# Optimization experiments

Hardware: AMD Instinct MI355X
Metric: run time of the kernel (lower is better)

The kernel has to match this reference:

```python
import jax, jax.numpy as jnp
import numpy as np

B, N, D, L = 4, 256, 512, 3  # batch, seq_len, input_dim, n_layer


def setup_inputs() -> dict:
    key = jax.random.key(0)
    ks = jax.random.split(key, 12)
    s = 0.02
    return {
        "x": jax.random.normal(ks[0], (B, N, D), dtype=jnp.float32),
        # Highway: L layers, each a gate Linear(D,D) and transform Linear(D,D)
        "hw_gate_w": jax.random.normal(ks[1], (L, D, D), dtype=jnp.float32) * s,
        "hw_gate_b": jnp.zeros((L, D), dtype=jnp.float32),
        "hw_tr_w": jax.random.normal(ks[2], (L, D, D), dtype=jnp.float32) * s,
        "hw_tr_b": jnp.zeros((L, D), dtype=jnp.float32),
        # link_weight MLP: Linear(2D,D) -> ReLU -> [Linear(D,D) -> ReLU]*(L-2) -> Linear(D,1) -> Sigmoid
        "lw0_w": jax.random.normal(ks[3], (D, 2 * D), dtype=jnp.float32) * s,
        "lw0_b": jnp.zeros((D,), dtype=jnp.float32),
        "lw1_w": jax.random.normal(ks[4], (D, D), dtype=jnp.float32) * s,
        "lw1_b": jnp.zeros((D,), dtype=jnp.float32),
        "lwo_w": jax.random.normal(ks[5], (1, D), dtype=jnp.float32) * s,
        "lwo_b": jnp.zeros((1,), dtype=jnp.float32),
    }


def _highway(x, gw, gb, tw, tb):
    # standard highway: y = g * relu(Wt x + bt) + (1 - g) * x, g = sigmoid(Wg x + bg)
    for i in range(gw.shape[0]):
        g = jax.nn.sigmoid(jnp.einsum('bnd,ed->bne', x, gw[i]) + gb[i])
        t = jax.nn.relu(jnp.einsum('bnd,ed->bne', x, tw[i]) + tb[i])
        x = g * t + (1.0 - g) * x
    return x


def reference(x, hw_gate_w, hw_gate_b, hw_tr_w, hw_tr_b,
              lw0_w, lw0_b, lw1_w, lw1_b, lwo_w, lwo_b):
    d = x.shape[-1]
    h = _highway(x, hw_gate_w, hw_gate_b, hw_tr_w, hw_tr_b)  # [B,N,D]
    # Fused pairwise-concat + first Linear: cat(h_i, h_j) @ W0.T ==
    # h_i @ W0[:, :D].T + h_j @ W0[:, D:].T  (avoids the [B,N*N,2D] tensor)
    a = jnp.einsum('bnd,ed->bne', h, lw0_w[:, :d])  # uses m1 (row i)
    b = jnp.einsum('bnd,ed->bne', h, lw0_w[:, d:])  # uses m2 (col j)
    z = jax.nn.relu(a[:, :, None, :] + b[:, None, :, :] + lw0_b)  # [B,N,N,D]
    # (dropout is identity in eval mode)
    z = jax.nn.relu(jnp.einsum('bijd,ed->bije', z, lw1_w) + lw1_b)  # n_layer-2 == 1 hidden layer
    out = jax.nn.sigmoid(jnp.einsum('bijd,d->bij', z, lwo_w[0]) + lwo_b[0])
    return out  # [B,N,N]
```

## Files before the change

### kernel.cpp

```cpp
#include <hip/hip_runtime.h>
#include <hip/hip_bf16.h>

#define BB 4
#define NN 256
#define DD 512

using short8   = __attribute__((ext_vector_type(8))) short;
using f32x4    = __attribute__((ext_vector_type(4))) float;
using uint32x4 = __attribute__((ext_vector_type(4))) unsigned int;

__device__ __forceinline__ unsigned short f2bf(float f) {
    unsigned int u = __float_as_uint(f);
    unsigned int r = (u + 0x7fffu + ((u >> 16) & 1u)) >> 16;
    return (unsigned short)r;
}

__device__ __forceinline__ unsigned cvtpk(float lo, float hi) {
    unsigned r;
    asm("v_cvt_pk_bf16_f32 %0, %1, %2" : "=v"(r) : "v"(lo), "v"(hi));
    return r;
}

template <int ROWS, int NW>
__device__ __forceinline__ void stage_rows(const unsigned short* src, int stride,
                                           short* dst, int tid) {
    int wave = tid >> 6, lane = tid & 63;
#pragma unroll
    for (int c = 0; c < ROWS / (8 * NW); ++c) {
        int rbase = (c * NW + wave) * 8;
        int row   = rbase + (lane >> 3);
        int slot  = (lane & 7) ^ (row & 7);
        const unsigned short* g = src + (size_t)row * stride + slot * 8;
        __builtin_amdgcn_global_load_lds(
            (const __attribute__((address_space(1))) void*)g,
            (__attribute__((address_space(3))) void*)(dst + rbase * 64),
            16, 0, 0);
    }
}

__device__ __forceinline__ short8 read_frag(const short* T, int rowBase, int k2) {
    int lane = threadIdx.x & 63;
    int row  = rowBase + (lane & 15);
    int slot = ((k2 * 4) + (lane >> 4)) ^ (row & 7);
    return *(const short8*)(T + row * 64 + slot * 8);
}

__global__ void prep_kernel(const float* __restrict__ x,
                            const float* __restrict__ gw, const float* __restrict__ tw,
                            const float* __restrict__ w0, const float* __restrict__ w1,
                            float* __restrict__ h0_f32, unsigned short* __restrict__ h0_bf,
                            unsigned short* __restrict__ wg_bf, unsigned short* __restrict__ wt_bf,
                            unsigned short* __restrict__ w0c_bf, unsigned short* __restrict__ w1_bf) {
    const int S_X = BB * NN * DD;
    const int S_W = 3 * DD * DD;
    const int S_W0 = 2 * DD * DD;
    const int S_W1 = DD * DD;
    int total = S_X + S_W + S_W + S_W0 + S_W1;
    for (int idx = blockIdx.x * blockDim.x + threadIdx.x; idx < total;
         idx += gridDim.x * blockDim.x) {
        int t = idx;
        if (t < S_X) { float v = x[t]; h0_f32[t] = v; h0_bf[t] = f2bf(v); continue; }
        t -= S_X;
        if (t < S_W) { wg_bf[t] = f2bf(gw[t]); continue; }
        t -= S_W;
        if (t < S_W) { wt_bf[t] = f2bf(tw[t]); continue; }
        t -= S_W;
        if (t < S_W0) {
            int e = t >> 9, d = t & 511;
            float v = (e < DD) ? w0[e * (2 * DD) + d] : w0[(e - DD) * (2 * DD) + DD + d];
            w0c_bf[t] = f2bf(v); continue;
        }
        t -= S_W0;
        w1_bf[t] = f2bf(w1[t]);
    }
}

__global__ __launch_bounds__(256) void highway_kernel(
        const float* __restrict__ h_in, const unsigned short* __restrict__ hbf_in,
        const unsigned short* __restrict__ wg_bf, const unsigned short* __restrict__ wt_bf,
        const float* __restrict__ gb, const float* __restrict__ tb,
        float* __restrict__ h_out, unsigned short* __restrict__ hbf_out) {
    __shared__ short ht[128 * 64];
    __shared__ short wgt[128 * 64];
    __shared__ short wtt[128 * 64];
    int tid = threadIdx.x, lane = tid & 63, wave = tid >> 6;
    int mt = blockIdx.x >> 2, et = blockIdx.x & 3;
    int m0 = mt * 128, e0 = et * 128;
    int wm = wave >> 1, we = wave & 1;
    f32x4 gacc[4][4] = {}, tacc[4][4] = {};
    for (int ks = 0; ks < 8; ++ks) {
        int d0 = ks * 64;
        __syncthreads();
        stage_rows<128, 4>(hbf_in + (size_t)m0 * DD + d0, DD, ht, tid);
        stage_rows<128, 4>(wg_bf + (size_t)e0 * DD + d0, DD, wgt, tid);
        stage_rows<128, 4>(wt_bf + (size_t)e0 * DD + d0, DD, wtt, tid);
        __syncthreads();
#pragma unroll
        for (int k2 = 0; k2 < 2; ++k2) {
            short8 af[4], bg[4], bt[4];
#pragma unroll
            for (int f = 0; f < 4; ++f) af[f] = read_frag(ht, wm * 64 + f * 16, k2);
#pragma unroll
            for (int f = 0; f < 4; ++f) bg[f] = read_frag(wgt, we * 64 + f * 16, k2);
#pragma unroll
            for (int f = 0; f < 4; ++f) bt[f] = read_frag(wtt, we * 64 + f * 16, k2);
#pragma unroll
            for (int fm = 0; fm < 4; ++fm)
#pragma unroll
                for (int fn = 0; fn < 4; ++fn) {
                    gacc[fm][fn] = __builtin_amdgcn_mfma_f32_16x16x32_bf16(af[fm], bg[fn], gacc[fm][fn], 0, 0, 0);
                    tacc[fm][fn] = __builtin_amdgcn_mfma_f32_16x16x32_bf16(af[fm], bt[fn], tacc[fm][fn], 0, 0, 0);
                }
        }
    }
#pragma unroll
    for (int fm = 0; fm < 4; ++fm)
#pragma unroll
        for (int fn = 0; fn < 4; ++fn) {
            int e = e0 + we * 64 + fn * 16 + (lane & 15);
            float gbe = gb[e], tbe = tb[e];
#pragma unroll
            for (int r = 0; r < 4; ++r) {
                int m = m0 + wm * 64 + fm * 16 + (lane >> 4) * 4 + r;
                float g = 1.f / (1.f + __expf(-(gacc[fm][fn][r] + gbe)));
                float tv = tacc[fm][fn][r] + tbe; tv = tv > 0.f ? tv : 0.f;
                float ho = h_in[(size_t)m * DD + e];
                float hn = g * tv + (1.f - g) * ho;
                h_out[(size_t)m * DD + e] = hn;
                hbf_out[(size_t)m * DD + e] = f2bf(hn);
            }
        }
}

__global__ __launch_bounds__(256) void ab_kernel(
        const unsigned short* __restrict__ hbf, const unsigned short* __restrict__ w0c_bf,
        const float* __restrict__ lw0_b,
        float* __restrict__ a_out, float* __restrict__ b_out) {
    __shared__ short ht[128 * 64];
    __shared__ short wt_[128 * 64];
    int tid = threadIdx.x, lane = tid & 63, wave = tid >> 6;
    int mt = blockIdx.x >> 3, et = blockIdx.x & 7;
    int m0 = mt * 128, e0 = et * 128;
    int wm = wave >> 1, we = wave & 1;
    f32x4 acc[4][4] = {};
    for (int ks = 0; ks < 8; ++ks) {
        __syncthreads();
        stage_rows<128, 4>(hbf + (size_t)m0 * DD + ks * 64, DD, ht, tid);
        stage_rows<128, 4>(w0c_bf + (size_t)e0 * DD + ks * 64, DD, wt_, tid);
        __syncthreads();
#pragma unroll
        for (int k2 = 0; k2 < 2; ++k2) {
            short8 af[4], bf_[4];
#pragma unroll
            for (int f = 0; f < 4; ++f) af[f] = read_frag(ht, wm * 64 + f * 16, k2);
#pragma unroll
            for (int f = 0; f < 4; ++f) bf_[f] = read_frag(wt_, we * 64 + f * 16, k2);
#pragma unroll
            for (int fm = 0; fm < 4; ++fm)
#pragma unroll
                for (int fn = 0; fn < 4; ++fn)
                    acc[fm][fn] = __builtin_amdgcn_mfma_f32_16x16x32_bf16(af[fm], bf_[fn], acc[fm][fn], 0, 0, 0);
        }
    }
#pragma unroll
    for (int fm = 0; fm < 4; ++fm)
#pragma unroll
        for (int fn = 0; fn < 4; ++fn) {
            int e = e0 + we * 64 + fn * 16 + (lane & 15);
#pragma unroll
            for (int r = 0; r < 4; ++r) {
                int m = m0 + wm * 64 + fm * 16 + (lane >> 4) * 4 + r;
                float v = acc[fm][fn][r];
                if (e < DD) a_out[(size_t)m * DD + e] = v + lw0_b[e];
                else        b_out[(size_t)m * DD + (e - DD)] = v;
            }
        }
}


#define Z_LOADS(K)                                                            \
    {                                                                         \
        const int dl_ = (K) * 64 + s * 8;                                     \
        alo = *(const f32x4*)(arow + dl_);                                    \
        ahi = *(const f32x4*)(arow + dl_ + 4);                                \
        const float* b0_ = brow + (size_t)rr * DD + dl_;                      \
        const float* b1_ = brow + (size_t)(64 + rr) * DD + dl_;               \
        b0lo = *(const f32x4*)b0_; b0hi = *(const f32x4*)(b0_ + 4);           \
        b1lo = *(const f32x4*)b1_; b1hi = *(const f32x4*)(b1_ + 4);           \
    }

#define Z_MATH()                                                              \
    {                                                                         \
        zw0[0] = cvtpk(fmaxf(alo[0] + b0lo[0], 0.f), fmaxf(alo[1] + b0lo[1], 0.f)); \
        zw0[1] = cvtpk(fmaxf(alo[2] + b0lo[2], 0.f), fmaxf(alo[3] + b0lo[3], 0.f)); \
        zw0[2] = cvtpk(fmaxf(ahi[0] + b0hi[0], 0.f), fmaxf(ahi[1] + b0hi[1], 0.f)); \
        zw0[3] = cvtpk(fmaxf(ahi[2] + b0hi[2], 0.f), fmaxf(ahi[3] + b0hi[3], 0.f)); \
        zw1[0] = cvtpk(fmaxf(alo[0] + b1lo[0], 0.f), fmaxf(alo[1] + b1lo[1], 0.f)); \
        zw1[1] = cvtpk(fmaxf(alo[2] + b1lo[2], 0.f), fmaxf(alo[3] + b1lo[3], 0.f)); \
        zw1[2] = cvtpk(fmaxf(ahi[0] + b1hi[0], 0.f), fmaxf(ahi[1] + b1hi[1], 0.f)); \
        zw1[3] = cvtpk(fmaxf(ahi[2] + b1hi[2], 0.f), fmaxf(ahi[3] + b1hi[3], 0.f)); \
    }

#define Z_WRITE()                                                             \
    {                                                                         \
        *(uint32x4*)(zs + rr * 64 + ((s ^ (rr & 7)) * 8)) = zw0;              \
        const int r1_ = 64 + rr;                                              \
        *(uint32x4*)(zs + r1_ * 64 + ((s ^ (r1_ & 7)) * 8)) = zw1;            \
    }

__global__ __launch_bounds__(512, 2) void pair_kernel(
        const float* __restrict__ a_f32, const float* __restrict__ b_f32,
        const unsigned short* __restrict__ w1_bf,
        const float* __restrict__ lw1_b, const float* __restrict__ lwo_w,
        const float* __restrict__ lwo_b, float* __restrict__ out) {
    __shared__ short ws[2][512 * 64];
    __shared__ short zs[128 * 64];
    int tid = threadIdx.x, lane = tid & 63, wave = tid >> 6;
    int bid = blockIdx.x;
    int bb = bid >> 9, i = (bid >> 1) & 255, j0 = (bid & 1) * 128;
    const float* arow = a_f32 + (size_t)(bb * NN + i) * DD;
    const float* brow = b_f32 + (size_t)(bb * NN + j0) * DD;
    int s = tid & 7, rr = tid >> 3;
    int we = wave;

    f32x4 acc[8][4] = {};
    uint32x4 zw0, zw1;
    f32x4 alo, ahi, b0lo, b0hi, b1lo, b1hi;

    Z_LOADS(0)
    Z_MATH()
    stage_rows<512, 8>(w1_bf, DD, ws[0], tid);

#pragma unroll
    for (int k = 0; k < 8; ++k) {
        __builtin_amdgcn_s_barrier();
        __builtin_amdgcn_sched_barrier(0);
        Z_WRITE()
        if (k < 7) {
            Z_LOADS(k + 1)
            stage_rows<512, 8>(w1_bf + (size_t)(k + 1) * 64, DD, ws[(k + 1) & 1], tid);
        }
        asm volatile("s_waitcnt lgkmcnt(0)" ::: "memory");
        if (k < 7) asm volatile("s_waitcnt vmcnt(14)" ::: "memory");
        else       asm volatile("s_waitcnt vmcnt(0)" ::: "memory");
        __builtin_amdgcn_s_barrier();
        __builtin_amdgcn_sched_barrier(0);

        const short* wc = ws[k & 1];
#pragma unroll
        for (int k2 = 0; k2 < 2; ++k2) {
            short8 bfr[4];
#pragma unroll
            for (int f = 0; f < 4; ++f) bfr[f] = read_frag(wc, we * 64 + f * 16, k2);
#pragma unroll
            for (int fh = 0; fh < 2; ++fh) {
                short8 af[4];
#pragma unroll
                for (int f = 0; f < 4; ++f) af[f] = read_frag(zs, (fh * 4 + f) * 16, k2);
#pragma unroll
                for (int fm = 0; fm < 4; ++fm)
#pragma unroll
                    for (int fn = 0; fn < 4; ++fn)
                        acc[fh * 4 + fm][fn] = __builtin_amdgcn_mfma_f32_16x16x32_bf16(
                            af[fm], bfr[fn], acc[fh * 4 + fm][fn], 0, 0, 0);
            }
        }
        if (k < 7) Z_MATH()
    }

    __syncthreads();
    float* s_red = (float*)zs;
#pragma unroll
    for (int fm = 0; fm < 8; ++fm) {
        float red[4] = {0.f, 0.f, 0.f, 0.f};
#pragma unroll
        for (int fn = 0; fn < 4; ++fn) {
            int e = we * 64 + fn * 16 + (lane & 15);
            float b1e = lw1_b[e], woe = lwo_w[e];
#pragma unroll
            for (int r = 0; r < 4; ++r) {
                float v = acc[fm][fn][r] + b1e;
                red[r] += (v > 0.f) ? v * woe : 0.f;
            }
        }
#pragma unroll
        for (int mask = 1; mask < 16; mask <<= 1)
#pragma unroll
            for (int r = 0; r < 4; ++r) red[r] += __shfl_xor(red[r], mask, 64);
        if ((lane & 15) == 0) {
#pragma unroll
            for (int r = 0; r < 4; ++r)
                s_red[we * 128 + fm * 16 + (lane >> 4) * 4 + r] = red[r];
        }
    }
    __syncthreads();
    if (tid < 128) {
        float v = lwo_b[0];
#pragma unroll
        for (int w8 = 0; w8 < 8; ++w8) v += s_red[w8 * 128 + tid];
        out[((size_t)(bb * NN + i)) * NN + j0 + tid] = 1.f / (1.f + __expf(-v));
    }
}

extern "C" void kernel_launch(void* const* d_in, const int* in_sizes, int n_in,
                              void* d_out, int out_size, void* d_ws, size_t ws_size,
                              hipStream_t stream) {
    const float* x    = (const float*)d_in[0];
    const float* gw   = (const float*)d_in[1];
    const float* gb   = (const float*)d_in[2];
    const float* tw   = (const float*)d_in[3];
    const float* tb   = (const float*)d_in[4];
    const float* w0   = (const float*)d_in[5];
    const float* w0b  = (const float*)d_in[6];
    const float* w1   = (const float*)d_in[7];
    const float* w1b_ = (const float*)d_in[8];
    const float* wo   = (const float*)d_in[9];
    const float* wob  = (const float*)d_in[10];
    float* out = (float*)d_out;

    char* w = (char*)d_ws;
    float* hA  = (float*)w;            w += (size_t)BB * NN * DD * 4;
    float* hB  = (float*)w;            w += (size_t)BB * NN * DD * 4;
    unsigned short* hbA = (unsigned short*)w; w += (size_t)BB * NN * DD * 2;
    unsigned short* hbB = (unsigned short*)w; w += (size_t)BB * NN * DD * 2;
    float* a_f = (float*)w;            w += (size_t)BB * NN * DD * 4;
    float* b_f = (float*)w;            w += (size_t)BB * NN * DD * 4;
    unsigned short* wg_bf  = (unsigned short*)w; w += (size_t)3 * DD * DD * 2;
    unsigned short* wt_bf  = (unsigned short*)w; w += (size_t)3 * DD * DD * 2;
    unsigned short* w0c_bf = (unsigned short*)w; w += (size_t)2 * DD * DD * 2;
    unsigned short* w1_bf  = (unsigned short*)w; w += (size_t)DD * DD * 2;

    prep_kernel<<<1024, 256, 0, stream>>>(x, gw, tw, w0, w1, hA, hbA, wg_bf, wt_bf, w0c_bf, w1_bf);

    highway_kernel<<<32, 256, 0, stream>>>(hA, hbA, wg_bf + 0 * DD * DD, wt_bf + 0 * DD * DD,
                                           gb + 0 * DD, tb + 0 * DD, hB, hbB);
    highway_kernel<<<32, 256, 0, stream>>>(hB, hbB, wg_bf + 1 * DD * DD, wt_bf + 1 * DD * DD,
                                           gb + 1 * DD, tb + 1 * DD, hA, hbA);
    highway_kernel<<<32, 256, 0, stream>>>(hA, hbA, wg_bf + 2 * DD * DD, wt_bf + 2 * DD * DD,
                                           gb + 2 * DD, tb + 2 * DD, hB, hbB);

    ab_kernel<<<64, 256, 0, stream>>>(hbB, w0c_bf, w0b, a_f, b_f);

    pair_kernel<<<2048, 512, 0, stream>>>(a_f, b_f, w1_bf, w1b_, wo, wob, out);
}
```

Before: 253.1 us.

## Double-buffer pair-kernel z tile, swizzle block order, shrink highway and ab tiles

Pair kernel now double-buffers the z tile in LDS. The next z chunk is written after the MFMA block, which removes one barrier per k-step, and s_setprio raises wave priority around the MFMAs. Blocks are remapped with a swizzle so neighbouring blocks land on different XCDs. The highway and ab GEMMs use smaller M/E tiles so they launch 128 blocks instead of 32/64, filling more CUs. The costs are more LDS per pair block, which may affect occupancy at 2 blocks per CU, and less data reuse per block in the small GEMMs.

```diff
diff --git a/kernel.cpp b/kernel.cpp
--- a/kernel.cpp
+++ b/kernel.cpp
@@ -80,48 +80,48 @@
         const unsigned short* __restrict__ wg_bf, const unsigned short* __restrict__ wt_bf,
         const float* __restrict__ gb, const float* __restrict__ tb,
         float* __restrict__ h_out, unsigned short* __restrict__ hbf_out) {
-    __shared__ short ht[128 * 64];
-    __shared__ short wgt[128 * 64];
-    __shared__ short wtt[128 * 64];
+    __shared__ short ht[64 * 64];
+    __shared__ short wgt[64 * 64];
+    __shared__ short wtt[64 * 64];
     int tid = threadIdx.x, lane = tid & 63, wave = tid >> 6;
-    int mt = blockIdx.x >> 2, et = blockIdx.x & 3;
-    int m0 = mt * 128, e0 = et * 128;
+    int mt = blockIdx.x >> 3, et = blockIdx.x & 7;
+    int m0 = mt * 64, e0 = et * 64;
     int wm = wave >> 1, we = wave & 1;
-    f32x4 gacc[4][4] = {}, tacc[4][4] = {};
+    f32x4 gacc[2][2] = {}, tacc[2][2] = {};
     for (int ks = 0; ks < 8; ++ks) {
         int d0 = ks * 64;
         __syncthreads();
-        stage_rows<128, 4>(hbf_in + (size_t)m0 * DD + d0, DD, ht, tid);
-        stage_rows<128, 4>(wg_bf + (size_t)e0 * DD + d0, DD, wgt, tid);
-        stage_rows<128, 4>(wt_bf + (size_t)e0 * DD + d0, DD, wtt, tid);
+        stage_rows<64, 4>(hbf_in + (size_t)m0 * DD + d0, DD, ht, tid);
+        stage_rows<64, 4>(wg_bf + (size_t)e0 * DD + d0, DD, wgt, tid);
+        stage_rows<64, 4>(wt_bf + (size_t)e0 * DD + d0, DD, wtt, tid);
         __syncthreads();
 #pragma unroll
         for (int k2 = 0; k2 < 2; ++k2) {
-            short8 af[4], bg[4], bt[4];
-#pragma unroll
-            for (int f = 0; f < 4; ++f) af[f] = read_frag(ht, wm * 64 + f * 16, k2);
-#pragma unroll
-            for (int f = 0; f < 4; ++f) bg[f] = read_frag(wgt, we * 64 + f * 16, k2);
-#pragma unroll
-            for (int f = 0; f < 4; ++f) bt[f] = read_frag(wtt, we * 64 + f * 16, k2);
-#pragma unroll
-            for (int fm = 0; fm < 4; ++fm)
-#pragma unroll
-                for (int fn = 0; fn < 4; ++fn) {
+            short8 af[2], bg[2], bt[2];
+#pragma unroll
+            for (int f = 0; f < 2; ++f) af[f] = read_frag(ht, wm * 32 + f * 16, k2);
+#pragma unroll
+            for (int f = 0; f < 2; ++f) bg[f] = read_frag(wgt, we * 32 + f * 16, k2);
+#pragma unroll
+            for (int f = 0; f < 2; ++f) bt[f] = read_frag(wtt, we * 32 + f * 16, k2);
+#pragma unroll
+            for (int fm = 0; fm < 2; ++fm)
+#pragma unroll
+                for (int fn = 0; fn < 2; ++fn) {
                     gacc[fm][fn] = __builtin_amdgcn_mfma_f32_16x16x32_bf16(af[fm], bg[fn], gacc[fm][fn], 0, 0, 0);
                     tacc[fm][fn] = __builtin_amdgcn_mfma_f32_16x16x32_bf16(af[fm], bt[fn], tacc[fm][fn], 0, 0, 0);
                 }
         }
     }
 #pragma unroll
-    for (int fm = 0; fm < 4; ++fm)
-#pragma unroll
-        for (int fn = 0; fn < 4; ++fn) {
-            int e = e0 + we * 64 + fn * 16 + (lane & 15);
+    for (int fm = 0; fm < 2; ++fm)
+#pragma unroll
+        for (int fn = 0; fn < 2; ++fn) {
+            int e = e0 + we * 32 + fn * 16 + (lane & 15);
             float gbe = gb[e], tbe = tb[e];
 #pragma unroll
             for (int r = 0; r < 4; ++r) {
-                int m = m0 + wm * 64 + fm * 16 + (lane >> 4) * 4 + r;
+                int m = m0 + wm * 32 + fm * 16 + (lane >> 4) * 4 + r;
                 float g = 1.f / (1.f + __expf(-(gacc[fm][fn][r] + gbe)));
                 float tv = tacc[fm][fn][r] + tbe; tv = tv > 0.f ? tv : 0.f;
                 float ho = h_in[(size_t)m * DD + e];
@@ -136,40 +136,40 @@
         const unsigned short* __restrict__ hbf, const unsigned short* __restrict__ w0c_bf,
         const float* __restrict__ lw0_b,
         float* __restrict__ a_out, float* __restrict__ b_out) {
-    __shared__ short ht[128 * 64];
+    __shared__ short ht[64 * 64];
     __shared__ short wt_[128 * 64];
     int tid = threadIdx.x, lane = tid & 63, wave = tid >> 6;
     int mt = blockIdx.x >> 3, et = blockIdx.x & 7;
-    int m0 = mt * 128, e0 = et * 128;
+    int m0 = mt * 64, e0 = et * 128;
     int wm = wave >> 1, we = wave & 1;
-    f32x4 acc[4][4] = {};
+    f32x4 acc[2][4] = {};
     for (int ks = 0; ks < 8; ++ks) {
         __syncthreads();
-        stage_rows<128, 4>(hbf + (size_t)m0 * DD + ks * 64, DD, ht, tid);
+        stage_rows<64, 4>(hbf + (size_t)m0 * DD + ks * 64, DD, ht, tid);
         stage_rows<128, 4>(w0c_bf + (size_t)e0 * DD + ks * 64, DD, wt_, tid);
         __syncthreads();
 #pragma unroll
         for (int k2 = 0; k2 < 2; ++k2) {
-            short8 af[4], bf_[4];
-#pragma unroll
-            for (int f = 0; f < 4; ++f) af[f] = read_frag(ht, wm * 64 + f * 16, k2);
+            short8 af[2], bf_[4];
+#pragma unroll
+            for (int f = 0; f < 2; ++f) af[f] = read_frag(ht, wm * 32 + f * 16, k2);
 #pragma unroll
             for (int f = 0; f < 4; ++f) bf_[f] = read_frag(wt_, we * 64 + f * 16, k2);
 #pragma unroll
-            for (int fm = 0; fm < 4; ++fm)
+            for (int fm = 0; fm < 2; ++fm)
 #pragma unroll
                 for (int fn = 0; fn < 4; ++fn)
                     acc[fm][fn] = __builtin_amdgcn_mfma_f32_16x16x32_bf16(af[fm], bf_[fn], acc[fm][fn], 0, 0, 0);
         }
     }
 #pragma unroll
-    for (int fm = 0; fm < 4; ++fm)
+    for (int fm = 0; fm < 2; ++fm)
 #pragma unroll
         for (int fn = 0; fn < 4; ++fn) {
             int e = e0 + we * 64 + fn * 16 + (lane & 15);
 #pragma unroll
             for (int r = 0; r < 4; ++r) {
-                int m = m0 + wm * 64 + fm * 16 + (lane >> 4) * 4 + r;
+                int m = m0 + wm * 32 + fm * 16 + (lane >> 4) * 4 + r;
                 float v = acc[fm][fn][r];
                 if (e < DD) a_out[(size_t)m * DD + e] = v + lw0_b[e];
                 else        b_out[(size_t)m * DD + (e - DD)] = v;
@@ -201,11 +201,11 @@
         zw1[3] = cvtpk(fmaxf(ahi[2] + b1hi[2], 0.f), fmaxf(ahi[3] + b1hi[3], 0.f)); \
     }
 
-#define Z_WRITE()                                                             \
+#define Z_WRITE(BUF)                                                          \
     {                                                                         \
-        *(uint32x4*)(zs + rr * 64 + ((s ^ (rr & 7)) * 8)) = zw0;              \
+        *(uint32x4*)((BUF) + rr * 64 + ((s ^ (rr & 7)) * 8)) = zw0;           \
         const int r1_ = 64 + rr;                                              \
-        *(uint32x4*)(zs + r1_ * 64 + ((s ^ (r1_ & 7)) * 8)) = zw1;            \
+        *(uint32x4*)((BUF) + r1_ * 64 + ((s ^ (r1_ & 7)) * 8)) = zw1;         \
     }
 
 __global__ __launch_bounds__(512, 2) void pair_kernel(
@@ -214,10 +214,11 @@
         const float* __restrict__ lw1_b, const float* __restrict__ lwo_w,
         const float* __restrict__ lwo_b, float* __restrict__ out) {
     __shared__ short ws[2][512 * 64];
-    __shared__ short zs[128 * 64];
+    __shared__ short zs[2][128 * 64];
     int tid = threadIdx.x, lane = tid & 63, wave = tid >> 6;
     int bid = blockIdx.x;
-    int bb = bid >> 9, i = (bid >> 1) & 255, j0 = (bid & 1) * 128;
+    int swz = (bid & 7) * 256 + (bid >> 3);
+    int bb = swz >> 9, i = (swz >> 1) & 255, j0 = (swz & 1) * 128;
     const float* arow = a_f32 + (size_t)(bb * NN + i) * DD;
     const float* brow = b_f32 + (size_t)(bb * NN + j0) * DD;
     int s = tid & 7, rr = tid >> 3;
@@ -228,25 +229,27 @@
     f32x4 alo, ahi, b0lo, b0hi, b1lo, b1hi;
 
     Z_LOADS(0)
+    stage_rows<512, 8>(w1_bf, DD, ws[0], tid);
     Z_MATH()
-    stage_rows<512, 8>(w1_bf, DD, ws[0], tid);
+    Z_WRITE(zs[0])
+    asm volatile("s_waitcnt lgkmcnt(0)" ::: "memory");
 
 #pragma unroll
     for (int k = 0; k < 8; ++k) {
         __builtin_amdgcn_s_barrier();
         __builtin_amdgcn_sched_barrier(0);
-        Z_WRITE()
         if (k < 7) {
             Z_LOADS(k + 1)
             stage_rows<512, 8>(w1_bf + (size_t)(k + 1) * 64, DD, ws[(k + 1) & 1], tid);
-        }
-        asm volatile("s_waitcnt lgkmcnt(0)" ::: "memory");
-        if (k < 7) asm volatile("s_waitcnt vmcnt(14)" ::: "memory");
-        else       asm volatile("s_waitcnt vmcnt(0)" ::: "memory");
-        __builtin_amdgcn_s_barrier();
+            asm volatile("s_waitcnt vmcnt(14)" ::: "memory");
+        } else {
+            asm volatile("s_waitcnt vmcnt(0)" ::: "memory");
+        }
         __builtin_amdgcn_sched_barrier(0);
 
+        const short* zc = zs[k & 1];
         const short* wc = ws[k & 1];
+        __builtin_amdgcn_s_setprio(1);
 #pragma unroll
         for (int k2 = 0; k2 < 2; ++k2) {
             short8 bfr[4];
@@ -256,7 +259,7 @@
             for (int fh = 0; fh < 2; ++fh) {
                 short8 af[4];
 #pragma unroll
-                for (int f = 0; f < 4; ++f) af[f] = read_frag(zs, (fh * 4 + f) * 16, k2);
+                for (int f = 0; f < 4; ++f) af[f] = read_frag(zc, (fh * 4 + f) * 16, k2);
 #pragma unroll
                 for (int fm = 0; fm < 4; ++fm)
 #pragma unroll
@@ -265,7 +268,13 @@
                             af[fm], bfr[fn], acc[fh * 4 + fm][fn], 0, 0, 0);
             }
         }
-        if (k < 7) Z_MATH()
+        __builtin_amdgcn_s_setprio(0);
+
+        if (k < 7) {
+            Z_MATH()
+            Z_WRITE(zs[(k + 1) & 1])
+            asm volatile("s_waitcnt lgkmcnt(0)" ::: "memory");
+        }
     }
 
     __syncthreads();
@@ -332,14 +341,14 @@
 
     prep_kernel<<<1024, 256, 0, stream>>>(x, gw, tw, w0, w1, hA, hbA, wg_bf, wt_bf, w0c_bf, w1_bf);
 
-    highway_kernel<<<32, 256, 0, stream>>>(hA, hbA, wg_bf + 0 * DD * DD, wt_bf + 0 * DD * DD,
-                                           gb + 0 * DD, tb + 0 * DD, hB, hbB);
-    highway_kernel<<<32, 256, 0, stream>>>(hB, hbB, wg_bf + 1 * DD * DD, wt_bf + 1 * DD * DD,
-                                           gb + 1 * DD, tb + 1 * DD, hA, hbA);
-    highway_kernel<<<32, 256, 0, stream>>>(hA, hbA, wg_bf + 2 * DD * DD, wt_bf + 2 * DD * DD,
-                                           gb + 2 * DD, tb + 2 * DD, hB, hbB);
-
-    ab_kernel<<<64, 256, 0, stream>>>(hbB, w0c_bf, w0b, a_f, b_f);
+    highway_kernel<<<128, 256, 0, stream>>>(hA, hbA, wg_bf + 0 * DD * DD, wt_bf + 0 * DD * DD,
+                                            gb + 0 * DD, tb + 0 * DD, hB, hbB);
+    highway_kernel<<<128, 256, 0, stream>>>(hB, hbB, wg_bf + 1 * DD * DD, wt_bf + 1 * DD * DD,
+                                            gb + 1 * DD, tb + 1 * DD, hA, hbA);
+    highway_kernel<<<128, 256, 0, stream>>>(hA, hbA, wg_bf + 2 * DD * DD, wt_bf + 2 * DD * DD,
+                                            gb + 2 * DD, tb + 2 * DD, hB, hbB);
+
+    ab_kernel<<<128, 256, 0, stream>>>(hbB, w0c_bf, w0b, a_f, b_f);
 
     pair_kernel<<<2048, 512, 0, stream>>>(a_f, b_f, w1_bf, w1b_, wo, wob, out);
 }
```

After: 220.3 us. 13.0% less time.
